# Kernel optimization log

Measured on AMD Instinct MI355X. Metric: run time of the kernel, lower is better.

The kernel has to match this reference:

```python
import jax, jax.numpy as jnp
import numpy as np
import math

NUM_WORDS = 8192
WORD_WIDTH = 512
PROJ_WIDTH = 64
NUM_HEADS = 8
SCALE_FACTOR = 100.0

def setup_inputs() -> dict:
    key = jax.random.key(0)
    kx, kq, kk, kv, ko = jax.random.split(key, 5)
    x = jax.random.normal(kx, (NUM_WORDS, WORD_WIDTH), dtype=jnp.float32)
    w_q = jax.random.normal(kq, (WORD_WIDTH, PROJ_WIDTH), dtype=jnp.float32) / SCALE_FACTOR
    w_k = jax.random.normal(kk, (WORD_WIDTH, PROJ_WIDTH), dtype=jnp.float32) / SCALE_FACTOR
    w_v = jax.random.normal(kv, (WORD_WIDTH, PROJ_WIDTH), dtype=jnp.float32) / SCALE_FACTOR
    w_o = jax.random.normal(ko, (WORD_WIDTH, WORD_WIDTH), dtype=jnp.float32)
    return {"x": x, "w_q": w_q, "w_k": w_k, "w_v": w_v, "w_o": w_o}

def reference(x, w_q, w_k, w_v, w_o):
    # Single self-attention head (all 8 heads in the source share the same weights).
    q = x @ w_q            # [N, P]
    k = x @ w_k            # [N, P]
    v = x @ w_v            # [N, P]
    scores = jax.nn.softmax((q @ k.T) / jnp.sqrt(jnp.float32(q.shape[1])), axis=1)  # [N, N]
    head = scores @ v      # [N, P]
    # concat of NUM_HEADS identical head outputs along dim=1
    concat = jnp.tile(head, (1, NUM_HEADS))  # [N, NUM_HEADS*P]
    return concat @ w_o    # [N, WORD_WIDTH]
```

## Files before the change

### kernel.cpp

```cpp
#include <hip/hip_runtime.h>
#include <stdint.h>

#define N_WORDS 8192
#define LOG2E_8 0.18033688011112043f

typedef __attribute__((ext_vector_type(8))) short short8;
typedef __attribute__((ext_vector_type(4))) float f32x4;
typedef __attribute__((ext_vector_type(16))) float f32x16;
typedef __attribute__((ext_vector_type(2))) __fp16 pkhalf2;
typedef __attribute__((ext_vector_type(4))) _Float16 half4;
typedef __attribute__((ext_vector_type(8))) _Float16 half8;

__device__ __forceinline__ unsigned short f32_to_bf16(float f) {
    union { float f; unsigned u; } v; v.f = f;
    unsigned u = v.u;
    return (unsigned short)((u + 0x7FFFu + ((u >> 16) & 1u)) >> 16);
}

__device__ __forceinline__ unsigned short f32_to_f16(float f) {
    union { _Float16 h; unsigned short u; } cv;
    cv.h = (_Float16)f;
    return cv.u;
}

__device__ __forceinline__ void async16(const void* g, void* l) {
    __builtin_amdgcn_global_load_lds(
        (const __attribute__((address_space(1))) unsigned int*)g,
        (__attribute__((address_space(3))) unsigned int*)l, 16, 0, 0);
}

__global__ __launch_bounds__(256) void qkv_gemm(
    const float* __restrict__ x,
    const float* __restrict__ wq, const float* __restrict__ wk,
    const float* __restrict__ wv, const float* __restrict__ wo,
    unsigned short* __restrict__ qB, unsigned short* __restrict__ kB,
    unsigned short* __restrict__ vH, unsigned short* __restrict__ weT)
{
    int t = threadIdx.x;
    int mat = blockIdx.y;

    if (mat == 3) {
        int i = blockIdx.x * 256 + t;
        int p = i >> 9;
        int j = i & 511;
        float s = 0.0f;
#pragma unroll
        for (int h = 0; h < 8; ++h) s += wo[(size_t)(h * 64 + p) * 512 + j];
        weT[(size_t)j * 64 + p] = f32_to_f16(s);
        return;
    }

    __shared__ __align__(16) unsigned short ldsX[64 * 72];
    __shared__ __align__(16) unsigned short ldsW[64 * 72];

    int mt = blockIdx.x;
    const float* w = (mat == 0) ? wq : (mat == 1) ? wk : wv;

    int wvid = t >> 6, lane = t & 63;
    int lq = lane & 15, quad = lane >> 4;

    f32x4 acc[4];
#pragma unroll
    for (int nt = 0; nt < 4; ++nt) acc[nt] = (f32x4){0.f, 0.f, 0.f, 0.f};

    float4 xr[4];
    float wr[16];
    int wn = t & 63, wkbs = (t >> 6) * 16;

    {
#pragma unroll
        for (int j2 = 0; j2 < 4; ++j2) {
            int i = t + j2 * 256;
            int row = i >> 4, c4 = (i & 15) * 4;
            xr[j2] = *(const float4*)(x + (size_t)(mt * 64 + row) * 512 + c4);
        }
#pragma unroll
        for (int kk = 0; kk < 16; ++kk)
            wr[kk] = w[(size_t)(wkbs + kk) * 64 + wn];
    }

    for (int kb = 0; kb < 8; ++kb) {
        __syncthreads();
#pragma unroll
        for (int j2 = 0; j2 < 4; ++j2) {
            int i = t + j2 * 256;
            int row = i >> 4, c4 = (i & 15) * 4;
            unsigned p0 = f32_to_bf16(xr[j2].x) | ((unsigned)f32_to_bf16(xr[j2].y) << 16);
            unsigned p1 = f32_to_bf16(xr[j2].z) | ((unsigned)f32_to_bf16(xr[j2].w) << 16);
            *(uint2*)(&ldsX[row * 72 + c4]) = make_uint2(p0, p1);
        }
#pragma unroll
        for (int kk = 0; kk < 16; kk += 2) {
            unsigned p = f32_to_bf16(wr[kk]) | ((unsigned)f32_to_bf16(wr[kk + 1]) << 16);
            *(unsigned*)(&ldsW[wn * 72 + wkbs + kk]) = p;
        }
        __syncthreads();

        if (kb < 7) {
            int k0 = (kb + 1) * 64;
#pragma unroll
            for (int j2 = 0; j2 < 4; ++j2) {
                int i = t + j2 * 256;
                int row = i >> 4, c4 = (i & 15) * 4;
                xr[j2] = *(const float4*)(x + (size_t)(mt * 64 + row) * 512 + k0 + c4);
            }
#pragma unroll
            for (int kk = 0; kk < 16; ++kk)
                wr[kk] = w[(size_t)(k0 + wkbs + kk) * 64 + wn];
        }

        int m = wvid * 16 + lq;
        short8 a0 = *(const short8*)(&ldsX[m * 72 + quad * 8]);
        short8 a1 = *(const short8*)(&ldsX[m * 72 + 32 + quad * 8]);
#pragma unroll
        for (int nt = 0; nt < 4; ++nt) {
            short8 b0 = *(const short8*)(&ldsW[(nt * 16 + lq) * 72 + quad * 8]);
            short8 b1 = *(const short8*)(&ldsW[(nt * 16 + lq) * 72 + 32 + quad * 8]);
            acc[nt] = __builtin_amdgcn_mfma_f32_16x16x32_bf16(a0, b0, acc[nt], 0, 0, 0);
            acc[nt] = __builtin_amdgcn_mfma_f32_16x16x32_bf16(a1, b1, acc[nt], 0, 0, 0);
        }
    }

    __syncthreads();
    unsigned short* ldsO = ldsX;
#pragma unroll
    for (int nt = 0; nt < 4; ++nt) {
#pragma unroll
        for (int r = 0; r < 4; ++r) {
            int lr = wvid * 16 + quad * 4 + r;
            int n = nt * 16 + lq;
            float v = acc[nt][r];
            int off;
            unsigned short u;
            if (mat == 0) {
                v *= LOG2E_8;
                int col = (((n >> 3) ^ (lr & 7)) << 3) | (n & 7);
                off = lr * 64 + col;
                u = f32_to_bf16(v);
            } else if (mat == 1) {
                int c2 = n >> 3, j = n & 7;
                off = (((lr >> 5) << 2) + (c2 >> 1)) * 512
                    + (((c2 & 1) << 5) + (lr & 31)) * 8 + j;
                u = f32_to_bf16(v);
            } else {
                int j2 = (lr & 3) | (((lr >> 3) & 1) << 2);
                off = ((((lr >> 5) << 1) + ((lr >> 4) & 1)) * 2 + (n >> 5)) * 512
                    + ((((lr >> 2) & 1) << 5) + (n & 31)) * 8 + j2;
                u = f32_to_f16(v);
            }
            ldsO[off] = u;
        }
    }
    __syncthreads();
    {
        unsigned short* dst = (mat == 0) ? qB : (mat == 1) ? kB : vH;
        const uint4* U = (const uint4*)ldsO;
        uint4* G = (uint4*)((char*)dst + (size_t)mt * 8192);
        G[t] = U[t];
        G[t + 256] = U[t + 256];
    }
}

__global__ __launch_bounds__(256) void attn_kernel(
    const unsigned short* __restrict__ qB,
    const unsigned short* __restrict__ kB,
    const unsigned short* __restrict__ vH,
    unsigned short* __restrict__ pOh, float* __restrict__ pl,
    int nk, int sshift)
{
    __shared__ __align__(16) unsigned short ldsK[2][128 * 64];
    __shared__ __align__(16) unsigned short ldsV[2][64 * 128];

    int t = threadIdx.x;
    int bid = blockIdx.x;
    int s = bid & ((1 << sshift) - 1);
    int qb = bid >> sshift;
    int wvid = t >> 6, lane = t & 63;
    int l31 = lane & 31, hi = lane >> 5;
    int mbase = qb * 128 + wvid * 32;
    int n0 = s * nk;

    short8 qf[4];
    {
        int qrow = mbase + l31;
        const unsigned short* qr = qB + (size_t)qrow * 64;
        int s7 = qrow & 7;
#pragma unroll
        for (int c = 0; c < 4; ++c)
            qf[c] = *(const short8*)(qr + (((2 * c + hi) ^ s7) << 3));
    }

    f32x16 zero16;
#pragma unroll
    for (int i = 0; i < 16; ++i) zero16[i] = 0.f;
    f32x16 oacc[2];
    oacc[0] = zero16;
    oacc[1] = zero16;
    float lsum = 0.f;

    auto stage = [&](int buf, int nb) {
        const char* gK = (const char*)kB + (size_t)(nb >> 7) * 16384;
        const char* gV = (const char*)vH + (size_t)(nb >> 7) * 16384;
#pragma unroll
        for (int i = 0; i < 4; ++i) {
            int L0 = (wvid * 4 + i) * 64;
            async16(gK + (size_t)(L0 + lane) * 16, (char*)ldsK[buf] + (size_t)L0 * 16);
            async16(gV + (size_t)(L0 + lane) * 16, (char*)ldsV[buf] + (size_t)L0 * 16);
        }
    };

    int tiles = nk >> 7;
    stage(0, n0);
    int cur = 0;

    for (int tt = 0; tt < tiles; ++tt) {
        __syncthreads();
        if (tt + 1 < tiles) stage(cur ^ 1, n0 + (tt + 1) * 128);

        __builtin_amdgcn_s_setprio(1);
        const char* Kb = (const char*)ldsK[cur] + (size_t)lane * 16;
        const char* Vb = (const char*)ldsV[cur] + (size_t)lane * 16;

#pragma unroll
        for (int nt = 0; nt < 4; ++nt) {
            f32x16 st = zero16;
#pragma unroll
            for (int c = 0; c < 4; ++c) {
                short8 a = *(const short8*)(Kb + (nt * 4 + c) * 1024);
                st = __builtin_amdgcn_mfma_f32_32x32x16_bf16(a, qf[c], st, 0, 0, 0);
            }

            union { half8 v8[2]; pkhalf2 v2[8]; } pa;
#pragma unroll
            for (int p = 0; p < 8; ++p) {
                float e0 = exp2f(st[2 * p]);
                float e1 = exp2f(st[2 * p + 1]);
                lsum += e0 + e1;
                pa.v2[p] = __builtin_amdgcn_cvt_pkrtz(e0, e1);
            }

#pragma unroll
            for (int m = 0; m < 2; ++m) {
#pragma unroll
                for (int vt = 0; vt < 2; ++vt) {
                    half8 vb = *(const half8*)(Vb + (((nt * 2 + m) * 2) + vt) * 1024);
                    oacc[vt] = __builtin_amdgcn_mfma_f32_32x32x16_f16(
                        pa.v8[m], vb, oacc[vt], 0, 0, 0);
                }
            }
        }
        __builtin_amdgcn_s_setprio(0);
        cur ^= 1;
    }

    lsum += __shfl_xor(lsum, 32);

    size_t obase = (size_t)s * N_WORDS;
    if (hi == 0) pl[obase + mbase + l31] = lsum;

    __syncthreads();
    unsigned short* ldsO = &ldsK[0][0];
#pragma unroll
    for (int vt = 0; vt < 2; ++vt)
#pragma unroll
        for (int r = 0; r < 16; ++r) {
            int lrow = wvid * 32 + (r & 3) + 8 * (r >> 2) + 4 * hi;
            ldsO[lrow * 64 + vt * 32 + l31] = f32_to_f16(oacc[vt][r]);
        }
    __syncthreads();
    {
        const uint4* U = (const uint4*)ldsO;
        uint4* G = (uint4*)(pOh + (obase + (size_t)qb * 128) * 64);
#pragma unroll
        for (int j = 0; j < 4; ++j)
            G[t + 256 * j] = U[t + 256 * j];
    }
}

__global__ __launch_bounds__(256) void out_kernel(
    const unsigned short* __restrict__ pOh, const float* __restrict__ pl,
    const unsigned short* __restrict__ weT, float* __restrict__ out, int S)
{
    __shared__ __align__(16) _Float16 ldsH[16 * 72];
    int t = threadIdx.x;
    int r0 = blockIdx.x * 16;
    const _Float16* pOf = (const _Float16*)pOh;

#pragma unroll
    for (int j = 0; j < 4; ++j) {
        int i = t + j * 256;
        int row = i >> 6, d = i & 63;
        float so = 0.f, sl = 0.f;
        for (int s = 0; s < S; ++s) {
            so += (float)pOf[((size_t)s * N_WORDS + r0 + row) * 64 + d];
            sl += pl[(size_t)s * N_WORDS + r0 + row];
        }
        ldsH[row * 72 + d] = (_Float16)(so / sl);
    }
    __syncthreads();

    int wv = t >> 6, lane = t & 63;
    int lq = lane & 15, quad = lane >> 4;

    half8 a0 = *(const half8*)(&ldsH[lq * 72 + quad * 8]);
    half8 a1 = *(const half8*)(&ldsH[lq * 72 + 32 + quad * 8]);
    const _Float16* wT = (const _Float16*)weT;

#pragma unroll
    for (int ntl = 0; ntl < 8; ++ntl) {
        int nt = wv * 8 + ntl;
        const _Float16* wrow = wT + (size_t)(nt * 16 + lq) * 64;
        half8 b0 = *(const half8*)(wrow + quad * 8);
        half8 b1 = *(const half8*)(wrow + 32 + quad * 8);
        f32x4 acc = (f32x4){0.f, 0.f, 0.f, 0.f};
        acc = __builtin_amdgcn_mfma_f32_16x16x32_f16(a0, b0, acc, 0, 0, 0);
        acc = __builtin_amdgcn_mfma_f32_16x16x32_f16(a1, b1, acc, 0, 0, 0);
#pragma unroll
        for (int r = 0; r < 4; ++r)
            out[(size_t)(r0 + quad * 4 + r) * 512 + nt * 16 + lq] = acc[r];
    }
}

extern "C" void kernel_launch(void* const* d_in, const int* in_sizes, int n_in,
                              void* d_out, int out_size, void* d_ws, size_t ws_size,
                              hipStream_t stream)
{
    const float* x  = (const float*)d_in[0];
    const float* wq = (const float*)d_in[1];
    const float* wk = (const float*)d_in[2];
    const float* wv = (const float*)d_in[3];
    const float* wo = (const float*)d_in[4];
    float* out = (float*)d_out;

    char* ws = (char*)d_ws;
    unsigned short* qB  = (unsigned short*)(ws);
    unsigned short* kB  = (unsigned short*)(ws + 1048576);
    unsigned short* vH  = (unsigned short*)(ws + 2097152);
    unsigned short* weT = (unsigned short*)(ws + 3145728);
    float* pl           = (float*)(ws + 3211264);
    unsigned short* pOh = (unsigned short*)(ws + 3735552);

    size_t base = 3735552;
    int S = (ws_size >= base + 8u * 1048576u) ? 8 : 4;
    int sshift = (S == 8) ? 3 : 2;
    int nk = N_WORDS / S;

    hipLaunchKernelGGL(qkv_gemm, dim3(128, 4), dim3(256), 0, stream,
                       x, wq, wk, wv, wo, qB, kB, vH, weT);
    hipLaunchKernelGGL(attn_kernel, dim3(64 * S), dim3(256), 0, stream,
                       qB, kB, vH, pOh, pl, nk, sshift);
    hipLaunchKernelGGL(out_kernel, dim3(512), dim3(256), 0, stream,
                       pOh, pl, weT, out, S);
}
```

Before: 125.7 us.

## Widen attention blocks to 256 query rows with a 4-deep K/V prefetch ring

The attention kernel now runs 512-thread blocks covering 256 query rows, so each K/V tile staged into LDS is reused by twice as many waves. The double buffer becomes a four-slot ring with three tiles prefetched ahead, and explicit vmcnt waits replace the plain per-tile sync so loads stay in flight across iterations. The cost is 128 KB of LDS per block, which allows only one block per CU, and half as many blocks in the grid. Latency hiding therefore depends on the deeper prefetch and on 8 waves per block.

```diff
diff --git a/kernel.cpp b/kernel.cpp
--- a/kernel.cpp
+++ b/kernel.cpp
@@ -161,15 +161,15 @@
     }
 }
 
-__global__ __launch_bounds__(256) void attn_kernel(
+__global__ __launch_bounds__(512, 2) void attn_kernel(
     const unsigned short* __restrict__ qB,
     const unsigned short* __restrict__ kB,
     const unsigned short* __restrict__ vH,
     unsigned short* __restrict__ pOh, float* __restrict__ pl,
     int nk, int sshift)
 {
-    __shared__ __align__(16) unsigned short ldsK[2][128 * 64];
-    __shared__ __align__(16) unsigned short ldsV[2][64 * 128];
+    __shared__ __align__(16) unsigned short ldsK[4][128 * 64];
+    __shared__ __align__(16) unsigned short ldsV[4][64 * 128];
 
     int t = threadIdx.x;
     int bid = blockIdx.x;
@@ -177,7 +177,7 @@
     int qb = bid >> sshift;
     int wvid = t >> 6, lane = t & 63;
     int l31 = lane & 31, hi = lane >> 5;
-    int mbase = qb * 128 + wvid * 32;
+    int mbase = qb * 256 + wvid * 32;
     int n0 = s * nk;
 
     short8 qf[4];
@@ -198,28 +198,39 @@
     oacc[1] = zero16;
     float lsum = 0.f;
 
-    auto stage = [&](int buf, int nb) {
+    auto stage = [&](int ti, int nb) {
+        int buf = ti & 3;
         const char* gK = (const char*)kB + (size_t)(nb >> 7) * 16384;
         const char* gV = (const char*)vH + (size_t)(nb >> 7) * 16384;
-#pragma unroll
-        for (int i = 0; i < 4; ++i) {
-            int L0 = (wvid * 4 + i) * 64;
-            async16(gK + (size_t)(L0 + lane) * 16, (char*)ldsK[buf] + (size_t)L0 * 16);
-            async16(gV + (size_t)(L0 + lane) * 16, (char*)ldsV[buf] + (size_t)L0 * 16);
-        }
+        async16(gK + ((size_t)(wvid * 64) + lane) * 16,
+                (char*)ldsK[buf] + (size_t)wvid * 1024);
+        async16(gK + ((size_t)(512 + wvid * 64) + lane) * 16,
+                (char*)ldsK[buf] + 8192 + (size_t)wvid * 1024);
+        async16(gV + ((size_t)(wvid * 64) + lane) * 16,
+                (char*)ldsV[buf] + (size_t)wvid * 1024);
+        async16(gV + ((size_t)(512 + wvid * 64) + lane) * 16,
+                (char*)ldsV[buf] + 8192 + (size_t)wvid * 1024);
     };
 
     int tiles = nk >> 7;
     stage(0, n0);
-    int cur = 0;
+    stage(1, n0 + 128);
+    stage(2, n0 + 256);
 
     for (int tt = 0; tt < tiles; ++tt) {
-        __syncthreads();
-        if (tt + 1 < tiles) stage(cur ^ 1, n0 + (tt + 1) * 128);
+        int rem = tiles - 1 - tt;
+        if (rem >= 2)      asm volatile("s_waitcnt vmcnt(8)" ::: "memory");
+        else if (rem == 1) asm volatile("s_waitcnt vmcnt(4)" ::: "memory");
+        else               asm volatile("s_waitcnt vmcnt(0)" ::: "memory");
+        __builtin_amdgcn_sched_barrier(0);
+        __builtin_amdgcn_s_barrier();
+        __builtin_amdgcn_sched_barrier(0);
+
+        if (tt + 3 < tiles) stage(tt + 3, n0 + (tt + 3) * 128);
 
         __builtin_amdgcn_s_setprio(1);
-        const char* Kb = (const char*)ldsK[cur] + (size_t)lane * 16;
-        const char* Vb = (const char*)ldsV[cur] + (size_t)lane * 16;
+        const char* Kb = (const char*)ldsK[tt & 3] + (size_t)lane * 16;
+        const char* Vb = (const char*)ldsV[tt & 3] + (size_t)lane * 16;
 
 #pragma unroll
         for (int nt = 0; nt < 4; ++nt) {
@@ -250,7 +261,6 @@
             }
         }
         __builtin_amdgcn_s_setprio(0);
-        cur ^= 1;
     }
 
     lsum += __shfl_xor(lsum, 32);
@@ -270,10 +280,10 @@
     __syncthreads();
     {
         const uint4* U = (const uint4*)ldsO;
-        uint4* G = (uint4*)(pOh + (obase + (size_t)qb * 128) * 64);
+        uint4* G = (uint4*)(pOh + (obase + (size_t)qb * 256) * 64);
 #pragma unroll
         for (int j = 0; j < 4; ++j)
-            G[t + 256 * j] = U[t + 256 * j];
+            G[t + 512 * j] = U[t + 512 * j];
     }
 }
 
@@ -344,10 +354,11 @@
     int S = (ws_size >= base + 8u * 1048576u) ? 8 : 4;
     int sshift = (S == 8) ? 3 : 2;
     int nk = N_WORDS / S;
+    int nqb = N_WORDS / 256;
 
     hipLaunchKernelGGL(qkv_gemm, dim3(128, 4), dim3(256), 0, stream,
                        x, wq, wk, wv, wo, qB, kB, vH, weT);
-    hipLaunchKernelGGL(attn_kernel, dim3(64 * S), dim3(256), 0, stream,
+    hipLaunchKernelGGL(attn_kernel, dim3(nqb * S), dim3(512), 0, stream,
                        qB, kB, vH, pOh, pl, nk, sshift);
     hipLaunchKernelGGL(out_kernel, dim3(512), dim3(256), 0, stream,
                        pOh, pl, weT, out, S);
```

New measurement: 124.9 us (median of 2 runs). Within noise of the previous version (-0.6%).
